# Optimization experiments

Hardware: AMD Instinct MI355X
Metric: run time of the kernel (lower is better)

## Reference

```python
import jax, jax.numpy as jnp
import numpy as np

B, S, E, H, L, NH, OUT = 32, 512, 512, 512, 2, 8, 1
HD = E // NH  # head dim


def setup_inputs() -> dict:
    key = jax.random.key(0)
    ks = jax.random.split(key, 16)
    sc_e = 1.0 / np.sqrt(E)
    sc_h = 1.0 / np.sqrt(H)
    inp = {
        "x": jax.random.normal(ks[0], (B, S, E), dtype=jnp.float32),
        "Wq": jax.random.normal(ks[1], (E, E), dtype=jnp.float32) * sc_e,
        "bq": jnp.zeros((E,), dtype=jnp.float32),
        "Wk": jax.random.normal(ks[2], (E, E), dtype=jnp.float32) * sc_e,
        "bk": jnp.zeros((E,), dtype=jnp.float32),
        "Wv": jax.random.normal(ks[3], (E, E), dtype=jnp.float32) * sc_e,
        "bv": jnp.zeros((E,), dtype=jnp.float32),
        "Wo": jax.random.normal(ks[4], (E, E), dtype=jnp.float32) * sc_e,
        "bo": jnp.zeros((E,), dtype=jnp.float32),
        # stacked RNN cell params (layer 0 input = E = H, so all layers share shape)
        "Wih": jax.random.normal(ks[5], (L, H, H), dtype=jnp.float32) * sc_h,
        "bih": jnp.zeros((L, H), dtype=jnp.float32),
        "Whh": jax.random.normal(ks[6], (L, H, H), dtype=jnp.float32) * sc_h,
        "bhh": jnp.zeros((L, H), dtype=jnp.float32),
        "Wfc": jax.random.normal(ks[7], (OUT, H), dtype=jnp.float32) * sc_h,
        "bfc": jnp.zeros((OUT,), dtype=jnp.float32),
    }
    return inp


def _forward(x, Wq, bq, Wk, bk, Wv, bv, Wo, bo, Wih, bih, Whh, bhh, Wfc, bfc):
    # Multi-head attention (self-attention, no mask; dropout = identity in eval)
    Q = (x @ Wq.T + bq).reshape(B, S, NH, HD)
    K = (x @ Wk.T + bk).reshape(B, S, NH, HD)
    V = (x @ Wv.T + bv).reshape(B, S, NH, HD)
    scores = jnp.einsum("bqhd,bkhd->bhqk", Q, K) / jnp.sqrt(jnp.float32(HD))
    attn = jax.nn.softmax(scores, axis=-1)
    ctx = jnp.einsum("bhqk,bkhd->bqhd", attn, V).reshape(B, S, E)
    atten_out = ctx @ Wo.T + bo  # [B, S, E]

    # Multi-layer Elman RNN scan over time; only last-step hidden is used.
    h0 = jnp.zeros((L, B, H), dtype=x.dtype)

    def step(h, x_t):
        inp = x_t
        new_h = []
        for i in range(L):
            inp = jnp.tanh(inp @ Wih[i].T + bih[i] + h[i] @ Whh[i].T + bhh[i])
            new_h.append(inp)
        return jnp.stack(new_h), None

    h_final, _ = jax.lax.scan(step, h0, jnp.swapaxes(atten_out, 0, 1))  # scan over S
    return h_final[-1] @ Wfc.T + bfc  # [B, OUT]


def reference(x, Wq, bq, Wk, bk, Wv, bv, Wo, bo, Wih, bih, Whh, bhh, Wfc, bfc):
    return _forward(x, Wq, bq, Wk, bk, Wv, bv, Wo, bo, Wih, bih, Whh, bhh, Wfc, bfc)
```

## Files before the change

### kernel.cpp

```cpp
#include <hip/hip_runtime.h>
#include <hip/hip_fp16.h>

#define B 32
#define S 512
#define E 512
#define H 512
#define NH 8
#define HD 64
#define POISON 0x7FC0DEADu

typedef _Float16 h16x8 __attribute__((ext_vector_type(8)));
typedef _Float16 h16x4 __attribute__((ext_vector_type(4)));
typedef float f32x4 __attribute__((ext_vector_type(4)));

__global__ __launch_bounds__(256) void cast_h(const float* __restrict__ src,
                                              _Float16* __restrict__ dst, int n4) {
    int i = blockIdx.x * 256 + threadIdx.x;
    const int stride = gridDim.x * 256;
    for (; i < n4; i += stride) {
        float4 v = ((const float4*)src)[i];
        h16x4 o;
        o[0] = (_Float16)v.x; o[1] = (_Float16)v.y;
        o[2] = (_Float16)v.z; o[3] = (_Float16)v.w;
        ((h16x4*)dst)[i] = o;
    }
}

template <int OMODE>
__global__ __launch_bounds__(256) void gemm_mfma(const _Float16* __restrict__ A,
                                                 const _Float16* __restrict__ W,
                                                 const float* __restrict__ bias,
                                                 void* __restrict__ Cout,
                                                 int M, int N, int K) {
    __shared__ __align__(16) _Float16 Als[128 * 32];
    __shared__ __align__(16) _Float16 Bls[128 * 32];
    const int tid = threadIdx.x;
    const int m0 = blockIdx.y * 128;
    const int n0 = blockIdx.x * 128;
    const int lane = tid & 63;
    const int w = tid >> 6;
    const int wm = w >> 1, wn = w & 1;
    f32x4 acc[4][4] = {};

    const int srow = tid >> 1;
    const int shalf = tid & 1;
    const _Float16* Ag = A + (size_t)(m0 + srow) * K + shalf * 16;
    const _Float16* Wg = W + (size_t)(n0 + srow) * K + shalf * 16;

    for (int k0 = 0; k0 < K; k0 += 32) {
        h16x8 a0 = *(const h16x8*)(Ag + k0);
        h16x8 a1 = *(const h16x8*)(Ag + k0 + 8);
        h16x8 b0 = *(const h16x8*)(Wg + k0);
        h16x8 b1 = *(const h16x8*)(Wg + k0 + 8);
        __syncthreads();
        *(h16x8*)&Als[srow * 32 + shalf * 16] = a0;
        *(h16x8*)&Als[srow * 32 + shalf * 16 + 8] = a1;
        *(h16x8*)&Bls[srow * 32 + shalf * 16] = b0;
        *(h16x8*)&Bls[srow * 32 + shalf * 16 + 8] = b1;
        __syncthreads();
        h16x8 af[4], bf[4];
#pragma unroll
        for (int mt = 0; mt < 4; ++mt)
            af[mt] = *(const h16x8*)&Als[(wm * 64 + mt * 16 + (lane & 15)) * 32 + (lane >> 4) * 8];
#pragma unroll
        for (int nt = 0; nt < 4; ++nt)
            bf[nt] = *(const h16x8*)&Bls[(wn * 64 + nt * 16 + (lane & 15)) * 32 + (lane >> 4) * 8];
#pragma unroll
        for (int mt = 0; mt < 4; ++mt)
#pragma unroll
            for (int nt = 0; nt < 4; ++nt)
                acc[mt][nt] = __builtin_amdgcn_mfma_f32_16x16x32_f16(af[mt], bf[nt], acc[mt][nt], 0, 0, 0);
    }

    float* Cf = (float*)Cout;
    _Float16* Ch = (_Float16*)Cout;
    const int colb = n0 + wn * 64 + (lane & 15);
    const int rowb = m0 + wm * 64 + ((lane >> 4) << 2);
#pragma unroll
    for (int mt = 0; mt < 4; ++mt) {
#pragma unroll
        for (int nt = 0; nt < 4; ++nt) {
            const int c = colb + nt * 16;
            const float bv = bias[c];
            if (OMODE == 2) {
                const int R0 = rowb + mt * 16;
                const int bb = R0 >> 9, s = R0 & 511, hh = c >> 6, d = c & 63;
                h16x4 pk;
#pragma unroll
                for (int j = 0; j < 4; ++j) pk[j] = (_Float16)(acc[mt][nt][j] + bv);
                *(h16x4*)&Ch[((size_t)(bb * 8 + hh) * 64 + d) * 512 + s] = pk;
            } else {
#pragma unroll
                for (int j = 0; j < 4; ++j) {
                    const int R = rowb + mt * 16 + j;
                    const float v = acc[mt][nt][j] + bv;
                    if (OMODE == 0) Cf[(size_t)R * N + c] = v;
                    else if (OMODE == 3) Cf[((size_t)(R & 511) * 32 + (R >> 9)) * N + c] = v;
                    else Ch[(size_t)R * N + c] = (_Float16)v;
                }
            }
        }
    }
}

__global__ __launch_bounds__(256) void attn_mfma(_Float16* __restrict__ Qb,
                                                 const _Float16* __restrict__ Kb,
                                                 const _Float16* __restrict__ Vt) {
    __shared__ __align__(16) _Float16 Qs[64 * 72];
    __shared__ __align__(16) _Float16 Ks[64 * 72];
    __shared__ __align__(16) _Float16 Vs[64 * 72];
    __shared__ __align__(16) _Float16 Ps[4 * 16 * 72];
    const int tid = threadIdx.x;
    const int lane = tid & 63;
    const int w = tid >> 6;
    const int qt = blockIdx.x & 7;
    const int h = (blockIdx.x >> 3) & 7;
    const int b = blockIdx.x >> 6;
    const size_t qrow0 = (size_t)b * 512 + qt * 64;
    const int col0 = h * 64;

    {
        const int r = tid >> 2;
        const int c0 = (tid & 3) << 4;
        const _Float16* gq = &Qb[(qrow0 + r) * 512 + col0 + c0];
        *(h16x8*)&Qs[r * 72 + c0] = *(const h16x8*)(gq);
        *(h16x8*)&Qs[r * 72 + c0 + 8] = *(const h16x8*)(gq + 8);
    }
    __syncthreads();
    h16x8 aq[2];
#pragma unroll
    for (int ks = 0; ks < 2; ++ks)
        aq[ks] = *(const h16x8*)&Qs[(w * 16 + (lane & 15)) * 72 + ks * 32 + (lane >> 4) * 8];

    float m[4] = {-1e30f, -1e30f, -1e30f, -1e30f};
    float l[4] = {0.f, 0.f, 0.f, 0.f};
    f32x4 acco[4] = {};

    for (int kt = 0; kt < 8; ++kt) {
        __syncthreads();
        {
            const int r = tid >> 2;
            const int c0 = (tid & 3) << 4;
            const _Float16* gk = &Kb[((size_t)b * 512 + kt * 64 + r) * 512 + col0 + c0];
            *(h16x8*)&Ks[r * 72 + c0] = *(const h16x8*)(gk);
            *(h16x8*)&Ks[r * 72 + c0 + 8] = *(const h16x8*)(gk + 8);
            const _Float16* gv = &Vt[((size_t)(b * 8 + h) * 64 + r) * 512 + kt * 64 + c0];
            *(h16x8*)&Vs[r * 72 + c0] = *(const h16x8*)(gv);
            *(h16x8*)&Vs[r * 72 + c0 + 8] = *(const h16x8*)(gv + 8);
        }
        __syncthreads();
        f32x4 accs[4] = {};
#pragma unroll
        for (int nt = 0; nt < 4; ++nt) {
#pragma unroll
            for (int ks = 0; ks < 2; ++ks) {
                h16x8 bk = *(const h16x8*)&Ks[(nt * 16 + (lane & 15)) * 72 + ks * 32 + (lane >> 4) * 8];
                accs[nt] = __builtin_amdgcn_mfma_f32_16x16x32_f16(aq[ks], bk, accs[nt], 0, 0, 0);
            }
        }
#pragma unroll
        for (int j = 0; j < 4; ++j) {
            float v = fmaxf(fmaxf(accs[0][j], accs[1][j]), fmaxf(accs[2][j], accs[3][j]));
#pragma unroll
            for (int o = 1; o < 16; o <<= 1) v = fmaxf(v, __shfl_xor(v, o, 64));
            const float mn = fmaxf(m[j], v);
            const float scl = __expf(0.125f * (m[j] - mn));
            m[j] = mn;
            l[j] *= scl;
#pragma unroll
            for (int nt2 = 0; nt2 < 4; ++nt2) acco[nt2][j] *= scl;
            float ps = 0.f;
            const int prow = ((lane >> 4) << 2) + j;
#pragma unroll
            for (int nt = 0; nt < 4; ++nt) {
                const float p = __expf(0.125f * (accs[nt][j] - mn));
                ps += p;
                Ps[w * 16 * 72 + prow * 72 + nt * 16 + (lane & 15)] = (_Float16)p;
            }
#pragma unroll
            for (int o = 1; o < 16; o <<= 1) ps += __shfl_xor(ps, o, 64);
            l[j] += ps;
        }
        __syncthreads();
#pragma unroll
        for (int ks2 = 0; ks2 < 2; ++ks2) {
            h16x8 pa = *(const h16x8*)&Ps[w * 16 * 72 + (lane & 15) * 72 + ks2 * 32 + (lane >> 4) * 8];
#pragma unroll
            for (int nt2 = 0; nt2 < 4; ++nt2) {
                h16x8 bv = *(const h16x8*)&Vs[(nt2 * 16 + (lane & 15)) * 72 + ks2 * 32 + (lane >> 4) * 8];
                acco[nt2] = __builtin_amdgcn_mfma_f32_16x16x32_f16(pa, bv, acco[nt2], 0, 0, 0);
            }
        }
    }
#pragma unroll
    for (int j = 0; j < 4; ++j) {
        const float inv = 1.0f / l[j];
        const size_t r = qrow0 + w * 16 + ((lane >> 4) << 2) + j;
#pragma unroll
        for (int nt2 = 0; nt2 < 4; ++nt2)
            Qb[r * 512 + col0 + nt2 * 16 + (lane & 15)] = (_Float16)(acco[nt2][j] * inv);
    }
}

__global__ __launch_bounds__(256) void fill_poison(uint4* __restrict__ p, int n) {
    const uint4 v = {POISON, POISON, POISON, POISON};
    int i = blockIdx.x * 256 + threadIdx.x;
    const int st = gridDim.x * 256;
    for (; i < n; i += st) p[i] = v;
}

__device__ __forceinline__ unsigned long long poll2(const unsigned* p) {
    unsigned long long v = __hip_atomic_load((const unsigned long long*)p,
                                             __ATOMIC_RELAXED, __HIP_MEMORY_SCOPE_AGENT);
    while ((unsigned)v == POISON || (unsigned)(v >> 32) == POISON) {
        __builtin_amdgcn_s_sleep(1);
        v = __hip_atomic_load((const unsigned long long*)p,
                              __ATOMIC_RELAXED, __HIP_MEMORY_SCOPE_AGENT);
    }
    return v;
}

__global__ __launch_bounds__(256) void rnn_persist(const float* __restrict__ pre,
                                                   const float* __restrict__ Whh,
                                                   const float* __restrict__ bhh,
                                                   unsigned* __restrict__ hbuf,
                                                   _Float16* __restrict__ hbuf_h) {
    __shared__ float hl[512];
    __shared__ float part[64][17];
    const int tid = threadIdx.x;
    const int b = blockIdx.x & 31;
    const int sl = blockIdx.x >> 5;
    const int jq = tid & 15, kg = tid >> 4;
    const int jbase = sl * 64, k0 = kg * 32;
    const int j64 = tid & 63;

    f32x4 w[32];
#pragma unroll
    for (int jj = 0; jj < 4; ++jj)
#pragma unroll
        for (int c = 0; c < 8; ++c)
            w[jj * 8 + c] = *(const f32x4*)&Whh[(size_t)(jbase + jq * 4 + jj) * 512 + k0 + c * 4];
#pragma unroll
    for (int i = 0; i < 32; ++i) asm volatile("" : "+v"(w[i]));

    const float bj = bhh[jbase + j64];

    for (int t = 0; t < S; ++t) {
        const float pv = pre[((size_t)t * 32 + b) * 512 + jbase + j64];
        float a0 = 0.f, a1 = 0.f, a2 = 0.f, a3 = 0.f;
        if (t > 0) {
            const unsigned long long v = poll2(hbuf + (size_t)(t - 1) * (B * H) + b * H + tid * 2);
            hl[tid * 2] = __uint_as_float((unsigned)v);
            hl[tid * 2 + 1] = __uint_as_float((unsigned)(v >> 32));
            __syncthreads();
            f32x4 hw[8];
#pragma unroll
            for (int c = 0; c < 8; ++c) hw[c] = *(const f32x4*)&hl[k0 + c * 4];
#pragma unroll
            for (int c = 0; c < 8; ++c) {
                a0 += w[0 * 8 + c][0] * hw[c][0] + w[0 * 8 + c][1] * hw[c][1]
                    + w[0 * 8 + c][2] * hw[c][2] + w[0 * 8 + c][3] * hw[c][3];
                a1 += w[1 * 8 + c][0] * hw[c][0] + w[1 * 8 + c][1] * hw[c][1]
                    + w[1 * 8 + c][2] * hw[c][2] + w[1 * 8 + c][3] * hw[c][3];
                a2 += w[2 * 8 + c][0] * hw[c][0] + w[2 * 8 + c][1] * hw[c][1]
                    + w[2 * 8 + c][2] * hw[c][2] + w[2 * 8 + c][3] * hw[c][3];
                a3 += w[3 * 8 + c][0] * hw[c][0] + w[3 * 8 + c][1] * hw[c][1]
                    + w[3 * 8 + c][2] * hw[c][2] + w[3 * 8 + c][3] * hw[c][3];
            }
        }
        part[jq * 4 + 0][kg] = a0;
        part[jq * 4 + 1][kg] = a1;
        part[jq * 4 + 2][kg] = a2;
        part[jq * 4 + 3][kg] = a3;
        __syncthreads();
        if (tid < 64) {
            float s2 = 0.f;
#pragma unroll
            for (int i = 0; i < 16; ++i) s2 += part[tid][i];
            s2 += bj + pv;
            s2 = fminf(fmaxf(s2, -15.f), 15.f);
            const float ex = __expf(2.f * s2);
            const float hval = (ex - 1.f) / (ex + 1.f);
            const size_t idx = (size_t)t * (B * H) + b * H + jbase + tid;
            __hip_atomic_store(&hbuf[idx], __float_as_uint(hval),
                               __ATOMIC_RELAXED, __HIP_MEMORY_SCOPE_AGENT);
            hbuf_h[idx] = (_Float16)hval;
        }
        __syncthreads();
    }
}

__global__ __launch_bounds__(64) void fc_out(const unsigned* __restrict__ hbits,
                                             const float* __restrict__ Wfc,
                                             const float* __restrict__ bfc,
                                             float* __restrict__ out) {
    int b = blockIdx.x;
    int t = threadIdx.x;
    float a = 0.f;
    for (int j = t; j < 512; j += 64) a += __uint_as_float(hbits[b * 512 + j]) * Wfc[j];
#pragma unroll
    for (int o = 32; o; o >>= 1) a += __shfl_down(a, o, 64);
    if (t == 0) out[b] = a + bfc[0];
}

extern "C" void kernel_launch(void* const* d_in, const int* in_sizes, int n_in,
                              void* d_out, int out_size, void* d_ws, size_t ws_size,
                              hipStream_t stream) {
    const float* x   = (const float*)d_in[0];
    const float* Wq  = (const float*)d_in[1];
    const float* bq  = (const float*)d_in[2];
    const float* Wk  = (const float*)d_in[3];
    const float* bk  = (const float*)d_in[4];
    const float* Wv  = (const float*)d_in[5];
    const float* bv  = (const float*)d_in[6];
    const float* Wo  = (const float*)d_in[7];
    const float* bo  = (const float*)d_in[8];
    const float* Wih = (const float*)d_in[9];
    const float* bih = (const float*)d_in[10];
    const float* Whh = (const float*)d_in[11];
    const float* bhh = (const float*)d_in[12];
    const float* Wfc = (const float*)d_in[13];
    const float* bfc = (const float*)d_in[14];
    float* out = (float*)d_out;
    char* base = (char*)d_ws;

    _Float16* xh   = (_Float16*)(base);
    unsigned* h0u  = (unsigned*)(base);
    _Float16* Qh   = (_Float16*)(base + ((size_t)32 << 20));
    _Float16* h0h  = (_Float16*)(base + ((size_t)32 << 20));
    _Float16* Kh   = (_Float16*)(base + ((size_t)48 << 20));
    unsigned* h1u  = (unsigned*)(base + ((size_t)48 << 20));
    _Float16* Vth  = (_Float16*)(base + ((size_t)64 << 20));
    float*    pre  = (float*)(base + ((size_t)80 << 20));
    _Float16* wgt  = (_Float16*)(base + ((size_t)112 << 20));
    const size_t WSZ = 512 * 512;

    cast_h<<<dim3(4096), dim3(256), 0, stream>>>(x, xh, (B * S * E) / 4);
    cast_h<<<dim3(256), dim3(256), 0, stream>>>(Wq, wgt + 0 * WSZ, WSZ / 4);
    cast_h<<<dim3(256), dim3(256), 0, stream>>>(Wk, wgt + 1 * WSZ, WSZ / 4);
    cast_h<<<dim3(256), dim3(256), 0, stream>>>(Wv, wgt + 2 * WSZ, WSZ / 4);
    cast_h<<<dim3(256), dim3(256), 0, stream>>>(Wo, wgt + 3 * WSZ, WSZ / 4);
    cast_h<<<dim3(256), dim3(256), 0, stream>>>(Wih, wgt + 4 * WSZ, WSZ / 4);
    cast_h<<<dim3(256), dim3(256), 0, stream>>>(Wih + WSZ, wgt + 5 * WSZ, WSZ / 4);

    const dim3 gg(4, 128), blk(256);
    gemm_mfma<1><<<gg, blk, 0, stream>>>(xh, wgt + 0 * WSZ, bq, Qh, B * S, E, E);
    gemm_mfma<1><<<gg, blk, 0, stream>>>(xh, wgt + 1 * WSZ, bk, Kh, B * S, E, E);
    gemm_mfma<2><<<gg, blk, 0, stream>>>(xh, wgt + 2 * WSZ, bv, Vth, B * S, E, E);
    attn_mfma<<<dim3(B * NH * 8), blk, 0, stream>>>(Qh, Kh, Vth);
    gemm_mfma<1><<<gg, blk, 0, stream>>>(Qh, wgt + 3 * WSZ, bo, Kh, B * S, E, E);
    gemm_mfma<3><<<gg, blk, 0, stream>>>(Kh, wgt + 4 * WSZ, bih, pre, B * S, H, E);

    fill_poison<<<dim3(1024), blk, 0, stream>>>((uint4*)base, (32 << 20) / 16);
    rnn_persist<<<dim3(256), blk, 0, stream>>>(pre, Whh, bhh, h0u, h0h);
    gemm_mfma<0><<<gg, blk, 0, stream>>>(h0h, wgt + 5 * WSZ, bih + 512, pre, B * S, H, H);
    fill_poison<<<dim3(1024), blk, 0, stream>>>((uint4*)(base + ((size_t)48 << 20)),
                                                (32 << 20) / 16);
    rnn_persist<<<dim3(256), blk, 0, stream>>>(pre, Whh + WSZ, bhh + 512, h1u, h0h);
    fc_out<<<dim3(32), dim3(64), 0, stream>>>(h1u + (size_t)511 * B * H, Wfc, bfc, out);
}
```

Measured before the change: 1.408 ms.

## Store recurrent weights as fp16 in LDS and reduce with shuffles and fdot2

The persistent RNN kernel now converts its 64-row slice of Whh to fp16 and keeps it in swizzled shared memory instead of fp32 registers. The hidden state is staged as fp16, and each thread accumulates with packed fp16 dot2 instructions. The shared-memory partial-sum array and one barrier per step are replaced by a 16-lane xor-shuffle reduction. This is meant to cut per-step latency on the serial recurrence and free registers. The cost is LDS bandwidth for weight reads on every step and lower precision in the recurrent matmul, which can accumulate over 512 steps.

```diff
diff --git a/kernel.cpp b/kernel.cpp
--- a/kernel.cpp
+++ b/kernel.cpp
@@ -11,7 +11,22 @@
 
 typedef _Float16 h16x8 __attribute__((ext_vector_type(8)));
 typedef _Float16 h16x4 __attribute__((ext_vector_type(4)));
+typedef _Float16 h16x2 __attribute__((ext_vector_type(2)));
 typedef float f32x4 __attribute__((ext_vector_type(4)));
+
+#if __has_builtin(__builtin_amdgcn_fdot2)
+__device__ __forceinline__ float dot2f(h16x2 a, h16x2 b, float c) {
+    return __builtin_amdgcn_fdot2(a, b, c, false);
+}
+#else
+__device__ __forceinline__ float dot2f(h16x2 a, h16x2 b, float c) {
+    return c + (float)a[0] * (float)b[0] + (float)a[1] * (float)b[1];
+}
+#endif
+
+__device__ __forceinline__ h16x2 pr(h16x8 v, int q) {
+    h16x2 r; r[0] = v[2 * q]; r[1] = v[2 * q + 1]; return r;
+}
 
 __global__ __launch_bounds__(256) void cast_h(const float* __restrict__ src,
                                               _Float16* __restrict__ dst, int n4) {
@@ -220,68 +235,84 @@
     return v;
 }
 
-__global__ __launch_bounds__(256) void rnn_persist(const float* __restrict__ pre,
-                                                   const float* __restrict__ Whh,
-                                                   const float* __restrict__ bhh,
-                                                   unsigned* __restrict__ hbuf,
-                                                   _Float16* __restrict__ hbuf_h) {
-    __shared__ float hl[512];
-    __shared__ float part[64][17];
+__global__ __launch_bounds__(256, 1) void rnn_persist(const float* __restrict__ pre,
+                                                      const float* __restrict__ Whh,
+                                                      const float* __restrict__ bhh,
+                                                      unsigned* __restrict__ hbuf,
+                                                      _Float16* __restrict__ hbuf_h) {
+    __shared__ __align__(16) _Float16 Wl[64 * 512];
+    __shared__ __align__(16) _Float16 hlh[512];
     const int tid = threadIdx.x;
     const int b = blockIdx.x & 31;
     const int sl = blockIdx.x >> 5;
-    const int jq = tid & 15, kg = tid >> 4;
-    const int jbase = sl * 64, k0 = kg * 32;
-    const int j64 = tid & 63;
-
-    f32x4 w[32];
-#pragma unroll
-    for (int jj = 0; jj < 4; ++jj)
-#pragma unroll
-        for (int c = 0; c < 8; ++c)
-            w[jj * 8 + c] = *(const f32x4*)&Whh[(size_t)(jbase + jq * 4 + jj) * 512 + k0 + c * 4];
-#pragma unroll
-    for (int i = 0; i < 32; ++i) asm volatile("" : "+v"(w[i]));
-
-    const float bj = bhh[jbase + j64];
+    const int jq = tid >> 4;
+    const int kg = tid & 15;
+    const int jbase = sl * 64;
+    const int jloc = jq * 4 + (kg & 3);
+
+#pragma unroll
+    for (int i = 0; i < 16; ++i) {
+        const int e = tid + i * 256;
+        const int row = e >> 6;
+        const int blk = e & 63;
+        const float* src = Whh + (size_t)(jbase + row) * 512 + blk * 8;
+        float4 u0 = *(const float4*)src;
+        float4 u1 = *(const float4*)(src + 4);
+        h16x8 o;
+        o[0] = (_Float16)u0.x; o[1] = (_Float16)u0.y; o[2] = (_Float16)u0.z; o[3] = (_Float16)u0.w;
+        o[4] = (_Float16)u1.x; o[5] = (_Float16)u1.y; o[6] = (_Float16)u1.z; o[7] = (_Float16)u1.w;
+        const int bx = blk ^ ((blk >> 2) & 7);
+        *(h16x8*)&Wl[row * 512 + bx * 8] = o;
+    }
+    const float bj = bhh[jbase + jloc];
+    __syncthreads();
 
     for (int t = 0; t < S; ++t) {
-        const float pv = pre[((size_t)t * 32 + b) * 512 + jbase + j64];
-        float a0 = 0.f, a1 = 0.f, a2 = 0.f, a3 = 0.f;
+        const float pv = pre[((size_t)t * 32 + b) * 512 + jbase + jloc];
         if (t > 0) {
             const unsigned long long v = poll2(hbuf + (size_t)(t - 1) * (B * H) + b * H + tid * 2);
-            hl[tid * 2] = __uint_as_float((unsigned)v);
-            hl[tid * 2 + 1] = __uint_as_float((unsigned)(v >> 32));
-            __syncthreads();
-            f32x4 hw[8];
-#pragma unroll
-            for (int c = 0; c < 8; ++c) hw[c] = *(const f32x4*)&hl[k0 + c * 4];
-#pragma unroll
-            for (int c = 0; c < 8; ++c) {
-                a0 += w[0 * 8 + c][0] * hw[c][0] + w[0 * 8 + c][1] * hw[c][1]
-                    + w[0 * 8 + c][2] * hw[c][2] + w[0 * 8 + c][3] * hw[c][3];
-                a1 += w[1 * 8 + c][0] * hw[c][0] + w[1 * 8 + c][1] * hw[c][1]
-                    + w[1 * 8 + c][2] * hw[c][2] + w[1 * 8 + c][3] * hw[c][3];
-                a2 += w[2 * 8 + c][0] * hw[c][0] + w[2 * 8 + c][1] * hw[c][1]
-                    + w[2 * 8 + c][2] * hw[c][2] + w[2 * 8 + c][3] * hw[c][3];
-                a3 += w[3 * 8 + c][0] * hw[c][0] + w[3 * 8 + c][1] * hw[c][1]
-                    + w[3 * 8 + c][2] * hw[c][2] + w[3 * 8 + c][3] * hw[c][3];
-            }
-        }
-        part[jq * 4 + 0][kg] = a0;
-        part[jq * 4 + 1][kg] = a1;
-        part[jq * 4 + 2][kg] = a2;
-        part[jq * 4 + 3][kg] = a3;
-        __syncthreads();
-        if (tid < 64) {
-            float s2 = 0.f;
-#pragma unroll
-            for (int i = 0; i < 16; ++i) s2 += part[tid][i];
+            h16x2 hp;
+            hp[0] = (_Float16)__uint_as_float((unsigned)v);
+            hp[1] = (_Float16)__uint_as_float((unsigned)(v >> 32));
+            const int hb = tid >> 2;
+            const int hbx = hb ^ ((hb >> 2) & 7);
+            *(h16x2*)&hlh[hbx * 8 + (tid & 3) * 2] = hp;
+        }
+        __syncthreads();
+        float a[4] = {0.f, 0.f, 0.f, 0.f};
+        if (t > 0) {
+            h16x8 hw[4];
+#pragma unroll
+            for (int c = 0; c < 4; ++c) {
+                const int b8 = kg * 4 + c;
+                hw[c] = *(const h16x8*)&hlh[(b8 ^ (kg & 7)) * 8];
+            }
+#pragma unroll
+            for (int jj = 0; jj < 4; ++jj) {
+                const int j = jq * 4 + jj;
+                float s = 0.f;
+#pragma unroll
+                for (int c = 0; c < 4; ++c) {
+                    const int b8 = kg * 4 + c;
+                    h16x8 w8 = *(const h16x8*)&Wl[j * 512 + (b8 ^ (kg & 7)) * 8];
+#pragma unroll
+                    for (int q = 0; q < 4; ++q) s = dot2f(pr(w8, q), pr(hw[c], q), s);
+                }
+                a[jj] = s;
+            }
+        }
+#pragma unroll
+        for (int o = 1; o < 16; o <<= 1) {
+#pragma unroll
+            for (int jj = 0; jj < 4; ++jj) a[jj] += __shfl_xor(a[jj], o, 16);
+        }
+        if (kg < 4) {
+            float s2 = (kg == 0) ? a[0] : (kg == 1) ? a[1] : (kg == 2) ? a[2] : a[3];
             s2 += bj + pv;
             s2 = fminf(fmaxf(s2, -15.f), 15.f);
             const float ex = __expf(2.f * s2);
             const float hval = (ex - 1.f) / (ex + 1.f);
-            const size_t idx = (size_t)t * (B * H) + b * H + jbase + tid;
+            const size_t idx = (size_t)t * (B * H) + b * H + jbase + jloc;
             __hip_atomic_store(&hbuf[idx], __float_as_uint(hval),
                                __ATOMIC_RELAXED, __HIP_MEMORY_SCOPE_AGENT);
             hbuf_h[idx] = (_Float16)hval;
```

New measurement: 1.629 ms. +15.7%, slower.

## Rewrite RNN recurrence as 8-block MFMA kernel with counter-based step sync

Applied to the files above, without the earlier changes.

Replaces the 256-block fp32 persistent RNN, which polls poisoned hidden-state values per element, with an 8-block kernel. Each block holds a 64-column slice of Whh in fp16 shared memory and computes all 32 batch rows with MFMA. Blocks synchronize per time step through an acquire/release counter array, which removes the two large poison-fill passes and fp32 hidden buffers. The cost is fewer CUs in the serial loop, fp16 rounding of weights and hidden state, and a full 32x512 hidden reload from global memory every step.

```diff
diff --git a/kernel.cpp b/kernel.cpp
--- a/kernel.cpp
+++ b/kernel.cpp
@@ -7,7 +7,6 @@
 #define H 512
 #define NH 8
 #define HD 64
-#define POISON 0x7FC0DEADu
 
 typedef _Float16 h16x8 __attribute__((ext_vector_type(8)));
 typedef _Float16 h16x4 __attribute__((ext_vector_type(4)));
@@ -202,102 +201,100 @@
     }
 }
 
-__global__ __launch_bounds__(256) void fill_poison(uint4* __restrict__ p, int n) {
-    const uint4 v = {POISON, POISON, POISON, POISON};
+__global__ __launch_bounds__(256) void zero_ints(int* __restrict__ p, int n) {
     int i = blockIdx.x * 256 + threadIdx.x;
-    const int st = gridDim.x * 256;
-    for (; i < n; i += st) p[i] = v;
-}
-
-__device__ __forceinline__ unsigned long long poll2(const unsigned* p) {
-    unsigned long long v = __hip_atomic_load((const unsigned long long*)p,
-                                             __ATOMIC_RELAXED, __HIP_MEMORY_SCOPE_AGENT);
-    while ((unsigned)v == POISON || (unsigned)(v >> 32) == POISON) {
-        __builtin_amdgcn_s_sleep(1);
-        v = __hip_atomic_load((const unsigned long long*)p,
-                              __ATOMIC_RELAXED, __HIP_MEMORY_SCOPE_AGENT);
-    }
-    return v;
-}
-
-__global__ __launch_bounds__(256) void rnn_persist(const float* __restrict__ pre,
+    if (i < n) p[i] = 0;
+}
+
+__global__ __launch_bounds__(256, 1) void rnn_mfma(const float* __restrict__ pre,
                                                    const float* __restrict__ Whh,
                                                    const float* __restrict__ bhh,
-                                                   unsigned* __restrict__ hbuf,
-                                                   _Float16* __restrict__ hbuf_h) {
-    __shared__ float hl[512];
-    __shared__ float part[64][17];
+                                                   _Float16* __restrict__ hout,
+                                                   int* __restrict__ cnt) {
+    __shared__ __align__(16) _Float16 Wl[64 * 520];
+    __shared__ __align__(16) _Float16 hl[32 * 520];
     const int tid = threadIdx.x;
-    const int b = blockIdx.x & 31;
-    const int sl = blockIdx.x >> 5;
-    const int jq = tid & 15, kg = tid >> 4;
-    const int jbase = sl * 64, k0 = kg * 32;
-    const int j64 = tid & 63;
-
-    f32x4 w[32];
-#pragma unroll
-    for (int jj = 0; jj < 4; ++jj)
-#pragma unroll
-        for (int c = 0; c < 8; ++c)
-            w[jj * 8 + c] = *(const f32x4*)&Whh[(size_t)(jbase + jq * 4 + jj) * 512 + k0 + c * 4];
-#pragma unroll
-    for (int i = 0; i < 32; ++i) asm volatile("" : "+v"(w[i]));
-
-    const float bj = bhh[jbase + j64];
+    const int lane = tid & 63;
+    const int w = tid >> 6;
+    const int jbase = blockIdx.x * 64;
+    const int jc = jbase + w * 16 + (lane & 15);
+
+#pragma unroll
+    for (int i = 0; i < 16; ++i) {
+        const int e = tid + i * 256;
+        const int row = e >> 6;
+        const int c8 = e & 63;
+        const float* src = Whh + (size_t)(jbase + row) * 512 + c8 * 8;
+        float4 u0 = *(const float4*)src;
+        float4 u1 = *(const float4*)(src + 4);
+        h16x8 o;
+        o[0] = (_Float16)u0.x; o[1] = (_Float16)u0.y; o[2] = (_Float16)u0.z; o[3] = (_Float16)u0.w;
+        o[4] = (_Float16)u1.x; o[5] = (_Float16)u1.y; o[6] = (_Float16)u1.z; o[7] = (_Float16)u1.w;
+        *(h16x8*)&Wl[row * 520 + c8 * 8] = o;
+    }
+    const float bj = bhh[jc];
+    __syncthreads();
 
     for (int t = 0; t < S; ++t) {
-        const float pv = pre[((size_t)t * 32 + b) * 512 + jbase + j64];
-        float a0 = 0.f, a1 = 0.f, a2 = 0.f, a3 = 0.f;
+        float prv[2][4];
+#pragma unroll
+        for (int mt = 0; mt < 2; ++mt)
+#pragma unroll
+            for (int r = 0; r < 4; ++r) {
+                const int b = mt * 16 + ((lane >> 4) << 2) + r;
+                prv[mt][r] = pre[((size_t)t * 32 + b) * 512 + jc];
+            }
+        f32x4 acc0 = {}, acc1 = {};
         if (t > 0) {
-            const unsigned long long v = poll2(hbuf + (size_t)(t - 1) * (B * H) + b * H + tid * 2);
-            hl[tid * 2] = __uint_as_float((unsigned)v);
-            hl[tid * 2 + 1] = __uint_as_float((unsigned)(v >> 32));
+            while (__hip_atomic_load(&cnt[t - 1], __ATOMIC_ACQUIRE,
+                                     __HIP_MEMORY_SCOPE_AGENT) < 8) {
+                __builtin_amdgcn_s_sleep(2);
+            }
+            const _Float16* hsrc = hout + (size_t)(t - 1) * (B * H);
+#pragma unroll
+            for (int i = 0; i < 8; ++i) {
+                const int e = tid + i * 256;
+                const int row = e >> 6;
+                const int c8 = e & 63;
+                h16x8 v = *(const h16x8*)&hsrc[row * 512 + c8 * 8];
+                *(h16x8*)&hl[row * 520 + c8 * 8] = v;
+            }
             __syncthreads();
-            f32x4 hw[8];
-#pragma unroll
-            for (int c = 0; c < 8; ++c) hw[c] = *(const f32x4*)&hl[k0 + c * 4];
-#pragma unroll
-            for (int c = 0; c < 8; ++c) {
-                a0 += w[0 * 8 + c][0] * hw[c][0] + w[0 * 8 + c][1] * hw[c][1]
-                    + w[0 * 8 + c][2] * hw[c][2] + w[0 * 8 + c][3] * hw[c][3];
-                a1 += w[1 * 8 + c][0] * hw[c][0] + w[1 * 8 + c][1] * hw[c][1]
-                    + w[1 * 8 + c][2] * hw[c][2] + w[1 * 8 + c][3] * hw[c][3];
-                a2 += w[2 * 8 + c][0] * hw[c][0] + w[2 * 8 + c][1] * hw[c][1]
-                    + w[2 * 8 + c][2] * hw[c][2] + w[2 * 8 + c][3] * hw[c][3];
-                a3 += w[3 * 8 + c][0] * hw[c][0] + w[3 * 8 + c][1] * hw[c][1]
-                    + w[3 * 8 + c][2] * hw[c][2] + w[3 * 8 + c][3] * hw[c][3];
-            }
-        }
-        part[jq * 4 + 0][kg] = a0;
-        part[jq * 4 + 1][kg] = a1;
-        part[jq * 4 + 2][kg] = a2;
-        part[jq * 4 + 3][kg] = a3;
-        __syncthreads();
-        if (tid < 64) {
-            float s2 = 0.f;
-#pragma unroll
-            for (int i = 0; i < 16; ++i) s2 += part[tid][i];
-            s2 += bj + pv;
-            s2 = fminf(fmaxf(s2, -15.f), 15.f);
-            const float ex = __expf(2.f * s2);
-            const float hval = (ex - 1.f) / (ex + 1.f);
-            const size_t idx = (size_t)t * (B * H) + b * H + jbase + tid;
-            __hip_atomic_store(&hbuf[idx], __float_as_uint(hval),
-                               __ATOMIC_RELAXED, __HIP_MEMORY_SCOPE_AGENT);
-            hbuf_h[idx] = (_Float16)hval;
-        }
-        __syncthreads();
-    }
-}
-
-__global__ __launch_bounds__(64) void fc_out(const unsigned* __restrict__ hbits,
+#pragma unroll
+            for (int ks = 0; ks < 16; ++ks) {
+                h16x8 bfr = *(const h16x8*)&Wl[(w * 16 + (lane & 15)) * 520 + ks * 32 + (lane >> 4) * 8];
+                h16x8 a0 = *(const h16x8*)&hl[((lane & 15)) * 520 + ks * 32 + (lane >> 4) * 8];
+                h16x8 a1 = *(const h16x8*)&hl[(16 + (lane & 15)) * 520 + ks * 32 + (lane >> 4) * 8];
+                acc0 = __builtin_amdgcn_mfma_f32_16x16x32_f16(a0, bfr, acc0, 0, 0, 0);
+                acc1 = __builtin_amdgcn_mfma_f32_16x16x32_f16(a1, bfr, acc1, 0, 0, 0);
+            }
+        }
+#pragma unroll
+        for (int mt = 0; mt < 2; ++mt) {
+#pragma unroll
+            for (int r = 0; r < 4; ++r) {
+                const int b = mt * 16 + ((lane >> 4) << 2) + r;
+                float s2 = (mt ? acc1[r] : acc0[r]) + prv[mt][r] + bj;
+                s2 = fminf(fmaxf(s2, -15.f), 15.f);
+                const float ex = __expf(2.f * s2);
+                hout[((size_t)t * 32 + b) * 512 + jc] = (_Float16)((ex - 1.f) / (ex + 1.f));
+            }
+        }
+        __syncthreads();
+        if (tid == 0) {
+            __hip_atomic_fetch_add(&cnt[t], 1, __ATOMIC_RELEASE, __HIP_MEMORY_SCOPE_AGENT);
+        }
+    }
+}
+
+__global__ __launch_bounds__(64) void fc_out(const _Float16* __restrict__ hh,
                                              const float* __restrict__ Wfc,
                                              const float* __restrict__ bfc,
                                              float* __restrict__ out) {
     int b = blockIdx.x;
     int t = threadIdx.x;
     float a = 0.f;
-    for (int j = t; j < 512; j += 64) a += __uint_as_float(hbits[b * 512 + j]) * Wfc[j];
+    for (int j = t; j < 512; j += 64) a += (float)hh[b * 512 + j] * Wfc[j];
 #pragma unroll
     for (int o = 32; o; o >>= 1) a += __shfl_down(a, o, 64);
     if (t == 0) out[b] = a + bfc[0];
@@ -325,14 +322,14 @@
     char* base = (char*)d_ws;
 
     _Float16* xh   = (_Float16*)(base);
-    unsigned* h0u  = (unsigned*)(base);
     _Float16* Qh   = (_Float16*)(base + ((size_t)32 << 20));
     _Float16* h0h  = (_Float16*)(base + ((size_t)32 << 20));
     _Float16* Kh   = (_Float16*)(base + ((size_t)48 << 20));
-    unsigned* h1u  = (unsigned*)(base + ((size_t)48 << 20));
+    _Float16* h1h  = (_Float16*)(base + ((size_t)48 << 20));
     _Float16* Vth  = (_Float16*)(base + ((size_t)64 << 20));
     float*    pre  = (float*)(base + ((size_t)80 << 20));
     _Float16* wgt  = (_Float16*)(base + ((size_t)112 << 20));
+    int*      cnt  = (int*)(base + ((size_t)115 << 20));
     const size_t WSZ = 512 * 512;
 
     cast_h<<<dim3(4096), dim3(256), 0, stream>>>(x, xh, (B * S * E) / 4);
@@ -342,6 +339,7 @@
     cast_h<<<dim3(256), dim3(256), 0, stream>>>(Wo, wgt + 3 * WSZ, WSZ / 4);
     cast_h<<<dim3(256), dim3(256), 0, stream>>>(Wih, wgt + 4 * WSZ, WSZ / 4);
     cast_h<<<dim3(256), dim3(256), 0, stream>>>(Wih + WSZ, wgt + 5 * WSZ, WSZ / 4);
+    zero_ints<<<dim3(4), dim3(256), 0, stream>>>(cnt, 1024);
 
     const dim3 gg(4, 128), blk(256);
     gemm_mfma<1><<<gg, blk, 0, stream>>>(xh, wgt + 0 * WSZ, bq, Qh, B * S, E, E);
@@ -351,11 +349,8 @@
     gemm_mfma<1><<<gg, blk, 0, stream>>>(Qh, wgt + 3 * WSZ, bo, Kh, B * S, E, E);
     gemm_mfma<3><<<gg, blk, 0, stream>>>(Kh, wgt + 4 * WSZ, bih, pre, B * S, H, E);
 
-    fill_poison<<<dim3(1024), blk, 0, stream>>>((uint4*)base, (32 << 20) / 16);
-    rnn_persist<<<dim3(256), blk, 0, stream>>>(pre, Whh, bhh, h0u, h0h);
+    rnn_mfma<<<dim3(8), blk, 0, stream>>>(pre, Whh, bhh, h0h, cnt);
     gemm_mfma<0><<<gg, blk, 0, stream>>>(h0h, wgt + 5 * WSZ, bih + 512, pre, B * S, H, H);
-    fill_poison<<<dim3(1024), blk, 0, stream>>>((uint4*)(base + ((size_t)48 << 20)),
-                                                (32 << 20) / 16);
-    rnn_persist<<<dim3(256), blk, 0, stream>>>(pre, Whh + WSZ, bhh + 512, h1u, h0h);
-    fc_out<<<dim3(32), dim3(64), 0, stream>>>(h1u + (size_t)511 * B * H, Wfc, bfc, out);
-}
+    rnn_mfma<<<dim3(8), blk, 0, stream>>>(pre, Whh + WSZ, bhh + 512, h1h, cnt + 512);
+    fc_out<<<dim3(32), dim3(64), 0, stream>>>(h1h + (size_t)511 * B * H, Wfc, bfc, out);
+}
```

Measured after the change: 3.843 ms. 173% more time.
